# Kernel tuning notes

Hardware: AMD Instinct MI355X
Metric: run time of the kernel (lower is better)

The kernel has to match this reference:

```python
import jax, jax.numpy as jnp
import numpy as np

HEADS = 8


def setup_inputs() -> dict:
    key = jax.random.key(0)
    ks = jax.random.split(key, 12)
    B, H, W, C = 2, 128, 256, 256
    inner = C  # num_heads * dim_head = 8 * 32

    def p(k, shape):
        return jax.random.normal(k, shape, dtype=jnp.float32) * 0.02

    return {
        "x": jax.random.normal(ks[0], (B, H * W, C), dtype=jnp.float32),
        "Wq_h": p(ks[1], (C, inner)),
        "Wk_h": p(ks[2], (C, inner)),
        "Wv_h": p(ks[3], (C, inner)),
        "Wo_h": p(ks[4], (inner, C)),
        "bo_h": p(ks[5], (C,)),
        "Wq_w": p(ks[6], (C, inner)),
        "Wk_w": p(ks[7], (C, inner)),
        "Wv_w": p(ks[8], (C, inner)),
        "Wo_w": p(ks[9], (inner, C)),
        "bo_w": p(ks[10], (C,)),
        "h": H,
        "w": W,
    }


def reference(x, Wq_h, Wk_h, Wv_h, Wo_h, bo_h, Wq_w, Wk_w, Wv_w, Wo_w, bo_w, h, w):
    b, n, c = x.shape
    heads = HEADS
    d = Wq_h.shape[1] // heads  # dim_head
    scale = d ** -0.5
    xs = x.reshape(b, h, w, c)  # [B,H,W,C]

    def proj(Wm):
        # [B,H,W,heads,d]
        return (xs @ Wm).reshape(b, h, w, heads, d)

    # --- height-axis attention: each column attends across all rows ---
    q, k, v = proj(Wq_h), proj(Wk_h), proj(Wv_h)
    s = jnp.einsum('bxwnd,bywnd->bwnxy', q, k) * scale  # [B,W,heads,H,H]
    a = jax.nn.softmax(s, axis=-1)
    oh = jnp.einsum('bwnxy,bywnd->bxwnd', a, v).reshape(b, h, w, heads * d)
    oh = oh @ Wo_h + bo_h

    # --- width-axis attention: each row attends across all columns ---
    q, k, v = proj(Wq_w), proj(Wk_w), proj(Wv_w)
    s = jnp.einsum('bhxnd,bhynd->bhnxy', q, k) * scale  # [B,H,heads,W,W]
    a = jax.nn.softmax(s, axis=-1)
    ow = jnp.einsum('bhnxy,bhynd->bhxnd', a, v).reshape(b, h, w, heads * d)
    ow = ow @ Wo_w + bo_w

    return (oh + ow).reshape(b, n, c)
```

## Files before the change

### kernel.cpp

```cpp
#include <hip/hip_runtime.h>
#include <hip/hip_bf16.h>
#include <stdint.h>

typedef unsigned short u16;
typedef short bf16x8 __attribute__((ext_vector_type(8)));
typedef float f32x4  __attribute__((ext_vector_type(4)));
typedef float f32x16 __attribute__((ext_vector_type(16)));
typedef unsigned int u32x4 __attribute__((ext_vector_type(4)));

__device__ __forceinline__ u16 f2bf(float f) {
    uint32_t u = __builtin_bit_cast(uint32_t, f);
    u += 0x7fffu + ((u >> 16) & 1u);
    return (u16)(u >> 16);
}

#if __has_builtin(__builtin_amdgcn_exp2f)
#define EXP2(x) __builtin_amdgcn_exp2f(x)
#else
extern "C" __device__ float __ocml_native_exp2_f32(float);
#define EXP2(x) __ocml_native_exp2_f32(x)
#endif

#define MM 65536
#define CC 256

#define QSCALE (1.4426950408889634f * 0.17677669529663687f)

__device__ __forceinline__ int perm_h(int t) {
    return ((t >> 15) << 15) | ((t & 127) << 8) | ((t >> 7) & 255);
}


__global__ void prep_kernel(
    const float* __restrict__ Wq_h, const float* __restrict__ Wk_h, const float* __restrict__ Wv_h,
    const float* __restrict__ Wo_h, const float* __restrict__ bo_h,
    const float* __restrict__ Wq_w, const float* __restrict__ Wk_w, const float* __restrict__ Wv_w,
    const float* __restrict__ Wo_w, const float* __restrict__ bo_w,
    u16* __restrict__ Wh_t, u16* __restrict__ Ww_t,
    u16* __restrict__ Woh_t, u16* __restrict__ Wow_t,
    u16* __restrict__ Wocat, float* __restrict__ bias)
{
    const int tid = blockIdx.x * 256 + threadIdx.x;
    const int nth = gridDim.x * 256;

    for (int i = tid; i < 768 * 256; i += nth) {
        int n = i >> 8, kk = i & 255;
        int which = n >> 8, nn = n & 255;
        const float* Wsh = (which == 0) ? Wq_h : (which == 1) ? Wk_h : Wv_h;
        const float* Wsw = (which == 0) ? Wq_w : (which == 1) ? Wk_w : Wv_w;
        Wh_t[i] = f2bf(Wsh[kk * 256 + nn]);
        Ww_t[i] = f2bf(Wsw[kk * 256 + nn]);
    }
    for (int i = tid; i < 256 * 256; i += nth) {
        int n = i >> 8, k = i & 255;
        Woh_t[i] = f2bf(Wo_h[k * 256 + n]);
        Wow_t[i] = f2bf(Wo_w[k * 256 + n]);
    }
    for (int i = tid; i < 256 * 512; i += nth) {
        int n = i >> 9, k = i & 511;
        float v = (k < 256) ? Wo_h[k * 256 + n] : Wo_w[(k - 256) * 256 + n];
        Wocat[i] = f2bf(v);
    }
    for (int i = tid; i < 256; i += nth) bias[i] = bo_h[i] + bo_w[i];
}

__global__ __launch_bounds__(256) void xcvt_kernel(const float* __restrict__ x, u16* __restrict__ xb)
{
    int i = blockIdx.x * 256 + threadIdx.x;
    const int nth = gridDim.x * 256;
    const int total = MM * 256 / 8;
    for (; i < total; i += nth) {
        const float* ap = x + (size_t)i * 8;
        float4 f0 = *(const float4*)ap;
        float4 f1 = *(const float4*)(ap + 4);
        u16 o[8] = { f2bf(f0.x), f2bf(f0.y), f2bf(f0.z), f2bf(f0.w),
                     f2bf(f1.x), f2bf(f1.y), f2bf(f1.z), f2bf(f1.w) };
        *(int4*)(xb + (size_t)i * 8) = *(const int4*)o;
    }
}

template<int PH, int XB>
__global__ __launch_bounds__(256) void gemm_qk_kernel(
    const float* __restrict__ x, const u16* __restrict__ xb, const u16* __restrict__ Bt,
    u16* __restrict__ Qb, u16* __restrict__ Kb)
{
    constexpr int S = PH ? 128 : 256;
    constexpr int L = PH ? 7 : 8;
    const int K = 256;
    __shared__ u16 sh[128 * 128];
    u16* As = sh;
    u16* Bs = sh + 128 * 64;
    const int tid = threadIdx.x;
    const int lane = tid & 63, wave = tid >> 6;
    const int wm = wave & 1, wn = wave >> 1;
    const int l15 = lane & 15, lq = lane >> 4;

    const int id = blockIdx.x;
    const int xcd = id & 7, wq = id >> 3;
    const int mt = xcd * 64 + (wq >> 2), nt = wq & 3;
    const int m0 = mt * 128, n0 = nt * 128;

    f32x4 acc[4][4];
#pragma unroll
    for (int i = 0; i < 4; i++)
#pragma unroll
        for (int j = 0; j < 4; j++)
#pragma unroll
            for (int t = 0; t < 4; t++) acc[i][j][t] = 0.0f;

    for (int kt = 0; kt < K; kt += 64) {
        __syncthreads();
#pragma unroll
        for (int i = 0; i < 4; i++) {
            int cid = i * 256 + tid;
            int r = cid >> 3, sc = cid & 7;
            int gk = kt + ((sc ^ (r & 7)) << 3);
            int rm = PH ? perm_h(m0 + r) : (m0 + r);
            if constexpr (XB) {
                *(int4*)(As + (size_t)cid * 8) = *(const int4*)(xb + (size_t)rm * 256 + gk);
            } else {
                const float* ap = x + (size_t)rm * 256 + gk;
                float4 f0 = *(const float4*)ap;
                float4 f1 = *(const float4*)(ap + 4);
                u16 o[8] = { f2bf(f0.x), f2bf(f0.y), f2bf(f0.z), f2bf(f0.w),
                             f2bf(f1.x), f2bf(f1.y), f2bf(f1.z), f2bf(f1.w) };
                *(int4*)(As + (size_t)cid * 8) = *(const int4*)o;
            }
            *(int4*)(Bs + (size_t)cid * 8) = *(const int4*)(Bt + (size_t)(n0 + r) * K + gk);
        }
        __syncthreads();
#pragma unroll
        for (int ks = 0; ks < 2; ks++) {
            bf16x8 af[4], bfr[4];
#pragma unroll
            for (int i = 0; i < 4; i++) {
                int row = wm * 64 + i * 16 + l15;
                int ca  = ks * 4 + lq;
                af[i]  = *(const bf16x8*)(As + row * 64 + ((ca ^ (row & 7)) << 3));
                int nn  = wn * 64 + i * 16 + l15;
                bfr[i] = *(const bf16x8*)(Bs + nn * 64 + ((ca ^ (nn & 7)) << 3));
            }
#pragma unroll
            for (int i = 0; i < 4; i++)
#pragma unroll
                for (int j = 0; j < 4; j++)
                    acc[i][j] = __builtin_amdgcn_mfma_f32_16x16x32_bf16(af[i], bfr[j], acc[i][j], 0, 0, 0);
        }
    }

    const float scale = (nt < 2) ? (float)QSCALE : 1.0f;
    __syncthreads();
#pragma unroll
    for (int i = 0; i < 4; i++)
#pragma unroll
        for (int j = 0; j < 4; j++)
#pragma unroll
            for (int r = 0; r < 4; r++) {
                int row = wm * 64 + i * 16 + lq * 4 + r;
                int col = wn * 64 + j * 16 + l15;
                sh[row * 128 + (col ^ ((row & 7) << 3))] = f2bf(acc[i][j][r] * scale);
            }
    __syncthreads();

    u16* dstb = (nt < 2) ? Qb : Kb;
    const int head = (nt * 4 + wave) & 7;
    const int gi = m0 >> L;
    const int seqbase = m0 & (S - 1);
    u16* dst = dstb + ((size_t)(gi * 8 + head) * S + seqbase) * 32;
    const int ln_ = lane & 31, lh_ = lane >> 5;
#pragma unroll
    for (int qt = 0; qt < 4; qt++)
#pragma unroll
        for (int half = 0; half < 2; half++) {
            int row  = qt * 32 + ln_;
            int colb = wave * 32 + half * 16 + lh_ * 8;
            int4 v = *(const int4*)(sh + row * 128 + (colb ^ ((row & 7) << 3)));
            *(int4*)(dst + qt * 1024 + half * 512 + lane * 8) = v;
        }
}

template<int PH, int XB>
__global__ __launch_bounds__(256) void gemm_vt_kernel(
    const u16* __restrict__ Wt, const float* __restrict__ x, const u16* __restrict__ xb,
    u16* __restrict__ Vb)
{
    constexpr int S = PH ? 128 : 256;
    const int K = 256;
    __shared__ u16 sh[128 * 128];
    u16* As = sh;
    u16* Bs = sh + 128 * 64;
    const int tid = threadIdx.x;
    const int lane = tid & 63, wave = tid >> 6;
    const int wm = wave & 1, wn = wave >> 1;
    const int l15 = lane & 15, lq = lane >> 4;
    const int m0 = blockIdx.y * 128, n0 = blockIdx.x * 128;

    f32x4 acc[4][4];
#pragma unroll
    for (int i = 0; i < 4; i++)
#pragma unroll
        for (int j = 0; j < 4; j++)
#pragma unroll
            for (int t = 0; t < 4; t++) acc[i][j][t] = 0.0f;

    for (int kt = 0; kt < K; kt += 64) {
        __syncthreads();
#pragma unroll
        for (int i = 0; i < 4; i++) {
            int cid = i * 256 + tid;
            int r = cid >> 3, sc = cid & 7;
            int gk = kt + ((sc ^ (r & 7)) << 3);
            *(int4*)(As + (size_t)cid * 8) = *(const int4*)(Wt + (size_t)(m0 + r) * K + gk);
            int cm = PH ? perm_h(n0 + r) : (n0 + r);
            if constexpr (XB) {
                *(int4*)(Bs + (size_t)cid * 8) = *(const int4*)(xb + (size_t)cm * 256 + gk);
            } else {
                const float* bp = x + (size_t)cm * 256 + gk;
                float4 f0 = *(const float4*)bp;
                float4 f1 = *(const float4*)(bp + 4);
                u16 o[8] = { f2bf(f0.x), f2bf(f0.y), f2bf(f0.z), f2bf(f0.w),
                             f2bf(f1.x), f2bf(f1.y), f2bf(f1.z), f2bf(f1.w) };
                *(int4*)(Bs + (size_t)cid * 8) = *(const int4*)o;
            }
        }
        __syncthreads();
#pragma unroll
        for (int ks = 0; ks < 2; ks++) {
            bf16x8 af[4], bfr[4];
#pragma unroll
            for (int i = 0; i < 4; i++) {
                int row = wm * 64 + i * 16 + l15;
                int ca  = ks * 4 + lq;
                af[i]  = *(const bf16x8*)(As + row * 64 + ((ca ^ (row & 7)) << 3));
                int nn  = wn * 64 + i * 16 + l15;
                bfr[i] = *(const bf16x8*)(Bs + nn * 64 + ((ca ^ (nn & 7)) << 3));
            }
#pragma unroll
            for (int i = 0; i < 4; i++)
#pragma unroll
                for (int j = 0; j < 4; j++)
                    acc[i][j] = __builtin_amdgcn_mfma_f32_16x16x32_bf16(af[i], bfr[j], acc[i][j], 0, 0, 0);
        }
    }

    __syncthreads();
#pragma unroll
    for (int i = 0; i < 4; i++)
#pragma unroll
        for (int j = 0; j < 4; j++)
#pragma unroll
            for (int r = 0; r < 4; r++) {
                int row = wm * 64 + i * 16 + lq * 4 + r;
                int col = wn * 64 + j * 16 + l15;
                sh[row * 128 + (col ^ ((row & 7) << 3))] = f2bf(acc[i][j][r]);
            }
    __syncthreads();

    const int gi = n0 >> (PH ? 7 : 8);
    const int seqbase = n0 & (S - 1);
    const int head = (m0 >> 5) + wave;
    u16* dst = Vb + ((size_t)(gi * 8 + head) * S + seqbase) * 32;
    const int ln_ = lane & 31, lh_ = lane >> 5;
#pragma unroll
    for (int cl = 0; cl < 4; cl++)
#pragma unroll
        for (int half = 0; half < 2; half++) {
            int row  = wave * 32 + ln_;
            int colb = cl * 32 + half * 16 + lh_ * 8;
            int4 v = *(const int4*)(sh + row * 128 + (colb ^ ((row & 7) << 3)));
            *(int4*)(dst + cl * 1024 + half * 512 + lane * 8) = v;
        }
}

__global__ __launch_bounds__(256) void gemm_out_fused_kernel(
    const u16* __restrict__ Ah, const u16* __restrict__ Aw,
    const u16* __restrict__ Bcat, float* __restrict__ Cout, const float* __restrict__ bias)
{
    const int K = 512, N = 256;
    __shared__ u16 As[128 * 64];
    __shared__ u16 Bs[128 * 64];
    const int tid = threadIdx.x;
    const int lane = tid & 63, wave = tid >> 6;
    const int wm = wave & 1, wn = wave >> 1;
    const int l15 = lane & 15, lq = lane >> 4;

    const int id = blockIdx.x;
    const int xcd = id & 7, wq = id >> 3;
    const int mt = xcd * 64 + (wq >> 1), nt = wq & 1;
    const int m0 = mt * 128, n0 = nt * 128;

    f32x4 acc[4][4];
#pragma unroll
    for (int i = 0; i < 4; i++)
#pragma unroll
        for (int j = 0; j < 4; j++)
#pragma unroll
            for (int t = 0; t < 4; t++) acc[i][j][t] = 0.0f;

    for (int kt = 0; kt < K; kt += 64) {
        __syncthreads();
        const u16* Abase = (kt < 256) ? Ah : Aw;
        int koff = kt & 255;
#pragma unroll
        for (int i = 0; i < 4; i++) {
            int cid = i * 256 + tid;
            int r = cid >> 3, sc = cid & 7;
            int gs = (sc ^ (r & 7)) << 3;
            *(int4*)(As + (size_t)cid * 8) = *(const int4*)(Abase + (size_t)(m0 + r) * 256 + koff + gs);
            *(int4*)(Bs + (size_t)cid * 8) = *(const int4*)(Bcat + (size_t)(n0 + r) * K + kt + gs);
        }
        __syncthreads();
#pragma unroll
        for (int ks = 0; ks < 2; ks++) {
            bf16x8 af[4], bfr[4];
#pragma unroll
            for (int i = 0; i < 4; i++) {
                int row = wm * 64 + i * 16 + l15;
                int ca  = ks * 4 + lq;
                af[i]  = *(const bf16x8*)(As + row * 64 + ((ca ^ (row & 7)) << 3));
                int nn  = wn * 64 + i * 16 + l15;
                bfr[i] = *(const bf16x8*)(Bs + nn * 64 + ((ca ^ (nn & 7)) << 3));
            }
#pragma unroll
            for (int i = 0; i < 4; i++)
#pragma unroll
                for (int j = 0; j < 4; j++)
                    acc[i][j] = __builtin_amdgcn_mfma_f32_16x16x32_bf16(af[i], bfr[j], acc[i][j], 0, 0, 0);
        }
    }
#pragma unroll
    for (int i = 0; i < 4; i++)
#pragma unroll
        for (int j = 0; j < 4; j++)
#pragma unroll
            for (int r = 0; r < 4; r++) {
                int row = m0 + wm * 64 + i * 16 + lq * 4 + r;
                int col = n0 + wn * 64 + j * 16 + l15;
                Cout[(size_t)row * N + col] = acc[i][j][r] + bias[col];
            }
}

template<int MODE>
__global__ __launch_bounds__(256) void gemm_out_kernel(
    const u16* __restrict__ A16, const u16* __restrict__ Bt,
    float* __restrict__ Cout, const float* __restrict__ bias)
{
    const int K = 256, N = 256;
    __shared__ u16 As[128 * 64];
    __shared__ u16 Bs[128 * 64];
    const int tid = threadIdx.x;
    const int lane = tid & 63, wave = tid >> 6;
    const int wm = wave & 1, wn = wave >> 1;
    const int l15 = lane & 15, lq = lane >> 4;
    const int m0 = blockIdx.y * 128, n0 = blockIdx.x * 128;

    f32x4 acc[4][4];
#pragma unroll
    for (int i = 0; i < 4; i++)
#pragma unroll
        for (int j = 0; j < 4; j++)
#pragma unroll
            for (int t = 0; t < 4; t++) acc[i][j][t] = 0.0f;

    for (int kt = 0; kt < K; kt += 64) {
        __syncthreads();
#pragma unroll
        for (int i = 0; i < 4; i++) {
            int cid = i * 256 + tid;
            int r = cid >> 3, sc = cid & 7;
            int gk = kt + ((sc ^ (r & 7)) << 3);
            *(int4*)(As + (size_t)cid * 8) = *(const int4*)(A16 + (size_t)(m0 + r) * K + gk);
            *(int4*)(Bs + (size_t)cid * 8) = *(const int4*)(Bt + (size_t)(n0 + r) * K + gk);
        }
        __syncthreads();
#pragma unroll
        for (int ks = 0; ks < 2; ks++) {
            bf16x8 af[4], bfr[4];
#pragma unroll
            for (int i = 0; i < 4; i++) {
                int row = wm * 64 + i * 16 + l15;
                int ca  = ks * 4 + lq;
                af[i]  = *(const bf16x8*)(As + row * 64 + ((ca ^ (row & 7)) << 3));
                int nn  = wn * 64 + i * 16 + l15;
                bfr[i] = *(const bf16x8*)(Bs + nn * 64 + ((ca ^ (nn & 7)) << 3));
            }
#pragma unroll
            for (int i = 0; i < 4; i++)
#pragma unroll
                for (int j = 0; j < 4; j++)
                    acc[i][j] = __builtin_amdgcn_mfma_f32_16x16x32_bf16(af[i], bfr[j], acc[i][j], 0, 0, 0);
        }
    }
#pragma unroll
    for (int i = 0; i < 4; i++)
#pragma unroll
        for (int j = 0; j < 4; j++)
#pragma unroll
            for (int r = 0; r < 4; r++) {
                int row = m0 + wm * 64 + i * 16 + lq * 4 + r;
                int col = n0 + wn * 64 + j * 16 + l15;
                size_t idx = (size_t)row * N + col;
                if (MODE == 1) Cout[idx] = acc[i][j][r] + bias[col];
                else           Cout[idx] += acc[i][j][r];
            }
}

template<int S, int PH, int NT>
__global__ __launch_bounds__(NT) void attn_kernel(
    const u16* __restrict__ Qb, const u16* __restrict__ Kb,
    const u16* __restrict__ Vb, u16* __restrict__ att)
{
    constexpr int NC = S / 32;
    const int tid = threadIdx.x;
    const int lane = tid & 63;
    const int wave = tid >> 6;
    const int ln = lane & 31;
    const int lh = lane >> 5;

    const int bid = blockIdx.x;
    const int head = bid & 7;
    const int gi = bid >> 3;
    const int qs = wave * 32;
    const int g = gi * 8 + head;

    const u16* Qg = Qb + (size_t)g * S * 32;
    const u16* Kg = Kb + (size_t)g * S * 32;
    const u16* Vg = Vb + (size_t)g * S * 32;

    const u16* qp = Qg + (qs >> 5) * 1024 + lane * 8;
    bf16x8 bq0 = *(const bf16x8*)qp;
    bf16x8 bq1 = *(const bf16x8*)(qp + 512);

    f32x16 kz;
#pragma unroll
    for (int t = 0; t < 16; t++) kz[t] = 0.0f;
    asm("" : "+v"(kz));

    float rs[4] = {0.0f, 0.0f, 0.0f, 0.0f};
    f32x16 oacc;
#pragma unroll
    for (int t = 0; t < 16; t++) oacc[t] = 0.0f;

    const u16* kp0 = Kg + lane * 8;
    const u16* vp0 = Vg + lane * 8;
    bf16x8 ak0 = *(const bf16x8*)kp0;
    bf16x8 ak1 = *(const bf16x8*)(kp0 + 512);
    bf16x8 bv0 = *(const bf16x8*)vp0;
    bf16x8 bv1 = *(const bf16x8*)(vp0 + 512);

    for (int c = 0; c < NC; c++) {
        f32x16 z = __builtin_amdgcn_mfma_f32_32x32x16_bf16(ak0, bq0, kz, 0, 0, 0);
        z = __builtin_amdgcn_mfma_f32_32x32x16_bf16(ak1, bq1, z, 0, 0, 0);

        int cn = (c + 1 < NC) ? c + 1 : c;
        const u16* kp = kp0 + cn * 1024;
        const u16* vp = vp0 + cn * 1024;
        bf16x8 nk0 = *(const bf16x8*)kp;
        bf16x8 nk1 = *(const bf16x8*)(kp + 512);
        bf16x8 nv0 = *(const bf16x8*)vp;
        bf16x8 nv1 = *(const bf16x8*)(vp + 512);

        asm("" : "+v"(z));
        float p[16];
#pragma unroll
        for (int r = 0; r < 16; r++) { p[r] = EXP2(z[r]); rs[r & 3] += p[r]; }

        unsigned w[8];
#pragma unroll
        for (int t = 0; t < 8; t++) {
            unsigned d;
            asm("v_cvt_pk_bf16_f32 %0, %1, %2" : "=v"(d) : "v"(p[2 * t]), "v"(p[2 * t + 1]));
            w[t] = d;
        }
        auto s0 = __builtin_amdgcn_permlane32_swap(w[0], w[2], false, false);
        auto s1 = __builtin_amdgcn_permlane32_swap(w[1], w[3], false, false);
        auto s2 = __builtin_amdgcn_permlane32_swap(w[4], w[6], false, false);
        auto s3 = __builtin_amdgcn_permlane32_swap(w[5], w[7], false, false);
        u32x4 a0 = { (unsigned)s0[0], (unsigned)s1[0], (unsigned)s0[1], (unsigned)s1[1] };
        u32x4 a1 = { (unsigned)s2[0], (unsigned)s3[0], (unsigned)s2[1], (unsigned)s3[1] };
        bf16x8 pa0 = __builtin_bit_cast(bf16x8, a0);
        bf16x8 pa1 = __builtin_bit_cast(bf16x8, a1);

        oacc = __builtin_amdgcn_mfma_f32_32x32x16_bf16(pa0, bv0, oacc, 0, 0, 0);
        oacc = __builtin_amdgcn_mfma_f32_32x32x16_bf16(pa1, bv1, oacc, 0, 0, 0);

        ak0 = nk0; ak1 = nk1; bv0 = nv0; bv1 = nv1;
    }

    float rsum = (rs[0] + rs[1]) + (rs[2] + rs[3]);
    rsum += __shfl_xor(rsum, 32);
    float inv = 1.0f / rsum;
#pragma unroll
    for (int r = 0; r < 16; r++) {
        int row = (r & 3) + ((r >> 2) << 3) + (lh << 2);
        float is = __shfl(inv, row);
        int seq = qs + row;
        int m = PH ? ((gi >> 8) * 32768 + seq * 256 + (gi & 255))
                   : (gi * 256 + seq);
        att[(size_t)m * 256 + head * 32 + ln] = f2bf(oacc[r] * is);
    }
}

extern "C" void kernel_launch(void* const* d_in, const int* in_sizes, int n_in,
                              void* d_out, int out_size, void* d_ws, size_t ws_size,
                              hipStream_t stream)
{
    (void)in_sizes; (void)n_in; (void)out_size;
    const float* x    = (const float*)d_in[0];
    const float* Wq_h = (const float*)d_in[1];
    const float* Wk_h = (const float*)d_in[2];
    const float* Wv_h = (const float*)d_in[3];
    const float* Wo_h = (const float*)d_in[4];
    const float* bo_h = (const float*)d_in[5];
    const float* Wq_w = (const float*)d_in[6];
    const float* Wk_w = (const float*)d_in[7];
    const float* Wv_w = (const float*)d_in[8];
    const float* Wo_w = (const float*)d_in[9];
    const float* bo_w = (const float*)d_in[10];

    const size_t NB = (size_t)MM * 256;
    u16* Qb   = (u16*)d_ws;
    u16* Kb   = Qb + NB;
    u16* Vb   = Kb + NB;
    u16* attb = Vb + NB;
    u16* xb   = attb + NB;
    const size_t WT = (size_t)2 * 768 * 256 + (size_t)2 * 256 * 256 + (size_t)256 * 512 + 512;
    const bool use_xb = ws_size >= (5 * NB + WT) * sizeof(u16);
    u16* wp = use_xb ? (xb + NB) : xb;
    u16* Wh_t  = wp;
    u16* Ww_t  = Wh_t + 768 * 256;
    u16* Woh_t = Ww_t + 768 * 256;
    u16* Wow_t = Woh_t + 256 * 256;
    u16* Wocat = Wow_t + 256 * 256;
    float* bias = (float*)(Wocat + 256 * 512);

    prep_kernel<<<512, 256, 0, stream>>>(Wq_h, Wk_h, Wv_h, Wo_h, bo_h,
                                         Wq_w, Wk_w, Wv_w, Wo_w, bo_w,
                                         Wh_t, Ww_t, Woh_t, Wow_t, Wocat, bias);
    if (use_xb)
        xcvt_kernel<<<8192, 256, 0, stream>>>(x, xb);

    if (use_xb) {
        gemm_qk_kernel<1, 1><<<2048, 256, 0, stream>>>(x, xb, Wh_t, Qb, Kb);
        gemm_vt_kernel<1, 1><<<dim3(512, 2), 256, 0, stream>>>(Wh_t + 512 * 256, x, xb, Vb);
        attn_kernel<128, 1, 256><<<4096, 256, 0, stream>>>(Qb, Kb, Vb, attb);

        gemm_qk_kernel<0, 1><<<2048, 256, 0, stream>>>(x, xb, Ww_t, Qb, Kb);
        gemm_vt_kernel<0, 1><<<dim3(512, 2), 256, 0, stream>>>(Ww_t + 512 * 256, x, xb, Vb);
        attn_kernel<256, 0, 512><<<2048, 512, 0, stream>>>(Qb, Kb, Vb, xb);

        gemm_out_fused_kernel<<<1024, 256, 0, stream>>>(attb, xb, Wocat,
                                                        (float*)d_out, bias);
    } else {
        gemm_qk_kernel<1, 0><<<2048, 256, 0, stream>>>(x, xb, Wh_t, Qb, Kb);
        gemm_vt_kernel<1, 0><<<dim3(512, 2), 256, 0, stream>>>(Wh_t + 512 * 256, x, xb, Vb);
        attn_kernel<128, 1, 256><<<4096, 256, 0, stream>>>(Qb, Kb, Vb, attb);
        gemm_out_kernel<1><<<dim3(2, 512), 256, 0, stream>>>(attb, Woh_t, (float*)d_out, bias);

        gemm_qk_kernel<0, 0><<<2048, 256, 0, stream>>>(x, xb, Ww_t, Qb, Kb);
        gemm_vt_kernel<0, 0><<<dim3(512, 2), 256, 0, stream>>>(Ww_t + 512 * 256, x, xb, Vb);
        attn_kernel<256, 0, 512><<<2048, 512, 0, stream>>>(Qb, Kb, Vb, attb);
        gemm_out_kernel<2><<<dim3(2, 512), 256, 0, stream>>>(attb, Wow_t, (float*)d_out, nullptr);
    }
}
```

Measured before the change: 322.8 us.

## Double-buffer GEMM tiles with direct global-to-LDS async loads

In the QK, VT (bf16 input path) and fused output-projection GEMMs, tile staging now uses global_load_lds builtins that write 16-byte chunks straight into LDS, bypassing registers. Shared memory is double-buffered so the next K-tile is fetched while MFMAs run on the current one, with one barrier per iteration instead of two. This targets exposed global-load latency in these projection GEMMs. The cost is doubled LDS per block, which may lower occupancy, and correctness depends on the barrier covering completion of the asynchronous LDS writes.

```diff
diff --git a/kernel.cpp b/kernel.cpp
--- a/kernel.cpp
+++ b/kernel.cpp
@@ -20,6 +20,13 @@
 extern "C" __device__ float __ocml_native_exp2_f32(float);
 #define EXP2(x) __ocml_native_exp2_f32(x)
 #endif
+
+__device__ __forceinline__ void gl_lds16(const u16* g, u16* l) {
+    __builtin_amdgcn_global_load_lds(
+        (__attribute__((address_space(1))) void*)(g),
+        (__attribute__((address_space(3))) void*)(l),
+        16, 0, 0);
+}
 
 #define MM 65536
 #define CC 256
@@ -87,9 +94,7 @@
     constexpr int S = PH ? 128 : 256;
     constexpr int L = PH ? 7 : 8;
     const int K = 256;
-    __shared__ u16 sh[128 * 128];
-    u16* As = sh;
-    u16* Bs = sh + 128 * 64;
+    __shared__ u16 sh[XB ? 32768 : 16384];
     const int tid = threadIdx.x;
     const int lane = tid & 63, wave = tid >> 6;
     const int wm = wave & 1, wn = wave >> 1;
@@ -108,48 +113,74 @@
 #pragma unroll
             for (int t = 0; t < 4; t++) acc[i][j][t] = 0.0f;
 
-    for (int kt = 0; kt < K; kt += 64) {
+    auto mma_tile = [&](const u16* As, const u16* Bs) {
+#pragma unroll
+        for (int ks = 0; ks < 2; ks++) {
+            bf16x8 af[4], bfr[4];
+#pragma unroll
+            for (int i = 0; i < 4; i++) {
+                int row = wm * 64 + i * 16 + l15;
+                int ca  = ks * 4 + lq;
+                af[i]  = *(const bf16x8*)(As + row * 64 + ((ca ^ (row & 7)) << 3));
+                int nn  = wn * 64 + i * 16 + l15;
+                bfr[i] = *(const bf16x8*)(Bs + nn * 64 + ((ca ^ (nn & 7)) << 3));
+            }
+#pragma unroll
+            for (int i = 0; i < 4; i++)
+#pragma unroll
+                for (int j = 0; j < 4; j++)
+                    acc[i][j] = __builtin_amdgcn_mfma_f32_16x16x32_bf16(af[i], bfr[j], acc[i][j], 0, 0, 0);
+        }
+    };
+
+    if constexpr (XB) {
+        u16* As_[2] = { sh,        sh + 16384 };
+        u16* Bs_[2] = { sh + 8192, sh + 24576 };
+        auto stage = [&](int kt, int buf) {
+#pragma unroll
+            for (int i = 0; i < 4; i++) {
+                int cid = i * 256 + tid;
+                int r = cid >> 3, sc = cid & 7;
+                int gk = kt + ((sc ^ (r & 7)) << 3);
+                int rm = PH ? perm_h(m0 + r) : (m0 + r);
+                gl_lds16(xb + (size_t)rm * 256 + gk, As_[buf] + cid * 8);
+                gl_lds16(Bt + (size_t)(n0 + r) * K + gk, Bs_[buf] + cid * 8);
+            }
+        };
+        stage(0, 0);
         __syncthreads();
 #pragma unroll
-        for (int i = 0; i < 4; i++) {
-            int cid = i * 256 + tid;
-            int r = cid >> 3, sc = cid & 7;
-            int gk = kt + ((sc ^ (r & 7)) << 3);
-            int rm = PH ? perm_h(m0 + r) : (m0 + r);
-            if constexpr (XB) {
-                *(int4*)(As + (size_t)cid * 8) = *(const int4*)(xb + (size_t)rm * 256 + gk);
-            } else {
+        for (int t = 0; t < 4; t++) {
+            if (t + 1 < 4) stage((t + 1) * 64, (t + 1) & 1);
+            mma_tile(As_[t & 1], Bs_[t & 1]);
+            __syncthreads();
+        }
+    } else {
+        u16* As = sh;
+        u16* Bs = sh + 8192;
+        for (int kt = 0; kt < K; kt += 64) {
+            __syncthreads();
+#pragma unroll
+            for (int i = 0; i < 4; i++) {
+                int cid = i * 256 + tid;
+                int r = cid >> 3, sc = cid & 7;
+                int gk = kt + ((sc ^ (r & 7)) << 3);
+                int rm = PH ? perm_h(m0 + r) : (m0 + r);
                 const float* ap = x + (size_t)rm * 256 + gk;
                 float4 f0 = *(const float4*)ap;
                 float4 f1 = *(const float4*)(ap + 4);
                 u16 o[8] = { f2bf(f0.x), f2bf(f0.y), f2bf(f0.z), f2bf(f0.w),
                              f2bf(f1.x), f2bf(f1.y), f2bf(f1.z), f2bf(f1.w) };
                 *(int4*)(As + (size_t)cid * 8) = *(const int4*)o;
-            }
-            *(int4*)(Bs + (size_t)cid * 8) = *(const int4*)(Bt + (size_t)(n0 + r) * K + gk);
+                *(int4*)(Bs + (size_t)cid * 8) = *(const int4*)(Bt + (size_t)(n0 + r) * K + gk);
+            }
+            __syncthreads();
+            mma_tile(As, Bs);
         }
         __syncthreads();
-#pragma unroll
-        for (int ks = 0; ks < 2; ks++) {
-            bf16x8 af[4], bfr[4];
-#pragma unroll
-            for (int i = 0; i < 4; i++) {
-                int row = wm * 64 + i * 16 + l15;
-                int ca  = ks * 4 + lq;
-                af[i]  = *(const bf16x8*)(As + row * 64 + ((ca ^ (row & 7)) << 3));
-                int nn  = wn * 64 + i * 16 + l15;
-                bfr[i] = *(const bf16x8*)(Bs + nn * 64 + ((ca ^ (nn & 7)) << 3));
-            }
-#pragma unroll
-            for (int i = 0; i < 4; i++)
-#pragma unroll
-                for (int j = 0; j < 4; j++)
-                    acc[i][j] = __builtin_amdgcn_mfma_f32_16x16x32_bf16(af[i], bfr[j], acc[i][j], 0, 0, 0);
-        }
     }
 
     const float scale = (nt < 2) ? (float)QSCALE : 1.0f;
-    __syncthreads();
 #pragma unroll
     for (int i = 0; i < 4; i++)
 #pragma unroll
@@ -186,9 +217,7 @@
 {
     constexpr int S = PH ? 128 : 256;
     const int K = 256;
-    __shared__ u16 sh[128 * 128];
-    u16* As = sh;
-    u16* Bs = sh + 128 * 64;
+    __shared__ u16 sh[XB ? 32768 : 16384];
     const int tid = threadIdx.x;
     const int lane = tid & 63, wave = tid >> 6;
     const int wm = wave & 1, wn = wave >> 1;
@@ -203,18 +232,60 @@
 #pragma unroll
             for (int t = 0; t < 4; t++) acc[i][j][t] = 0.0f;
 
-    for (int kt = 0; kt < K; kt += 64) {
+    auto mma_tile = [&](const u16* As, const u16* Bs) {
+#pragma unroll
+        for (int ks = 0; ks < 2; ks++) {
+            bf16x8 af[4], bfr[4];
+#pragma unroll
+            for (int i = 0; i < 4; i++) {
+                int row = wm * 64 + i * 16 + l15;
+                int ca  = ks * 4 + lq;
+                af[i]  = *(const bf16x8*)(As + row * 64 + ((ca ^ (row & 7)) << 3));
+                int nn  = wn * 64 + i * 16 + l15;
+                bfr[i] = *(const bf16x8*)(Bs + nn * 64 + ((ca ^ (nn & 7)) << 3));
+            }
+#pragma unroll
+            for (int i = 0; i < 4; i++)
+#pragma unroll
+                for (int j = 0; j < 4; j++)
+                    acc[i][j] = __builtin_amdgcn_mfma_f32_16x16x32_bf16(af[i], bfr[j], acc[i][j], 0, 0, 0);
+        }
+    };
+
+    if constexpr (XB) {
+        u16* As_[2] = { sh,        sh + 16384 };
+        u16* Bs_[2] = { sh + 8192, sh + 24576 };
+        auto stage = [&](int kt, int buf) {
+#pragma unroll
+            for (int i = 0; i < 4; i++) {
+                int cid = i * 256 + tid;
+                int r = cid >> 3, sc = cid & 7;
+                int gk = kt + ((sc ^ (r & 7)) << 3);
+                gl_lds16(Wt + (size_t)(m0 + r) * K + gk, As_[buf] + cid * 8);
+                int cm = PH ? perm_h(n0 + r) : (n0 + r);
+                gl_lds16(xb + (size_t)cm * 256 + gk, Bs_[buf] + cid * 8);
+            }
+        };
+        stage(0, 0);
         __syncthreads();
 #pragma unroll
-        for (int i = 0; i < 4; i++) {
-            int cid = i * 256 + tid;
-            int r = cid >> 3, sc = cid & 7;
-            int gk = kt + ((sc ^ (r & 7)) << 3);
-            *(int4*)(As + (size_t)cid * 8) = *(const int4*)(Wt + (size_t)(m0 + r) * K + gk);
-            int cm = PH ? perm_h(n0 + r) : (n0 + r);
-            if constexpr (XB) {
-                *(int4*)(Bs + (size_t)cid * 8) = *(const int4*)(xb + (size_t)cm * 256 + gk);
-            } else {
+        for (int t = 0; t < 4; t++) {
+            if (t + 1 < 4) stage((t + 1) * 64, (t + 1) & 1);
+            mma_tile(As_[t & 1], Bs_[t & 1]);
+            __syncthreads();
+        }
+    } else {
+        u16* As = sh;
+        u16* Bs = sh + 8192;
+        for (int kt = 0; kt < K; kt += 64) {
+            __syncthreads();
+#pragma unroll
+            for (int i = 0; i < 4; i++) {
+                int cid = i * 256 + tid;
+                int r = cid >> 3, sc = cid & 7;
+                int gk = kt + ((sc ^ (r & 7)) << 3);
+                *(int4*)(As + (size_t)cid * 8) = *(const int4*)(Wt + (size_t)(m0 + r) * K + gk);
+                int cm = PH ? perm_h(n0 + r) : (n0 + r);
                 const float* bp = x + (size_t)cm * 256 + gk;
                 float4 f0 = *(const float4*)bp;
                 float4 f1 = *(const float4*)(bp + 4);
@@ -222,8 +293,86 @@
                              f2bf(f1.x), f2bf(f1.y), f2bf(f1.z), f2bf(f1.w) };
                 *(int4*)(Bs + (size_t)cid * 8) = *(const int4*)o;
             }
+            __syncthreads();
+            mma_tile(As, Bs);
         }
         __syncthreads();
+    }
+
+#pragma unroll
+    for (int i = 0; i < 4; i++)
+#pragma unroll
+        for (int j = 0; j < 4; j++)
+#pragma unroll
+            for (int r = 0; r < 4; r++) {
+                int row = wm * 64 + i * 16 + lq * 4 + r;
+                int col = wn * 64 + j * 16 + l15;
+                sh[row * 128 + (col ^ ((row & 7) << 3))] = f2bf(acc[i][j][r]);
+            }
+    __syncthreads();
+
+    const int gi = n0 >> (PH ? 7 : 8);
+    const int seqbase = n0 & (S - 1);
+    const int head = (m0 >> 5) + wave;
+    u16* dst = Vb + ((size_t)(gi * 8 + head) * S + seqbase) * 32;
+    const int ln_ = lane & 31, lh_ = lane >> 5;
+#pragma unroll
+    for (int cl = 0; cl < 4; cl++)
+#pragma unroll
+        for (int half = 0; half < 2; half++) {
+            int row  = wave * 32 + ln_;
+            int colb = cl * 32 + half * 16 + lh_ * 8;
+            int4 v = *(const int4*)(sh + row * 128 + (colb ^ ((row & 7) << 3)));
+            *(int4*)(dst + cl * 1024 + half * 512 + lane * 8) = v;
+        }
+}
+
+__global__ __launch_bounds__(256) void gemm_out_fused_kernel(
+    const u16* __restrict__ Ah, const u16* __restrict__ Aw,
+    const u16* __restrict__ Bcat, float* __restrict__ Cout, const float* __restrict__ bias)
+{
+    const int K = 512, N = 256;
+    __shared__ u16 sh[32768];
+    const int tid = threadIdx.x;
+    const int lane = tid & 63, wave = tid >> 6;
+    const int wm = wave & 1, wn = wave >> 1;
+    const int l15 = lane & 15, lq = lane >> 4;
+
+    const int id = blockIdx.x;
+    const int xcd = id & 7, wq = id >> 3;
+    const int mt = xcd * 64 + (wq >> 1), nt = wq & 1;
+    const int m0 = mt * 128, n0 = nt * 128;
+
+    f32x4 acc[4][4];
+#pragma unroll
+    for (int i = 0; i < 4; i++)
+#pragma unroll
+        for (int j = 0; j < 4; j++)
+#pragma unroll
+            for (int t = 0; t < 4; t++) acc[i][j][t] = 0.0f;
+
+    u16* As_[2] = { sh,        sh + 16384 };
+    u16* Bs_[2] = { sh + 8192, sh + 24576 };
+    auto stage = [&](int kt, int buf) {
+        const u16* Abase = (kt < 256) ? Ah : Aw;
+        int koff = kt & 255;
+#pragma unroll
+        for (int i = 0; i < 4; i++) {
+            int cid = i * 256 + tid;
+            int r = cid >> 3, sc = cid & 7;
+            int gs = (sc ^ (r & 7)) << 3;
+            gl_lds16(Abase + (size_t)(m0 + r) * 256 + koff + gs, As_[buf] + cid * 8);
+            gl_lds16(Bcat + (size_t)(n0 + r) * K + kt + gs, Bs_[buf] + cid * 8);
+        }
+    };
+
+    stage(0, 0);
+    __syncthreads();
+#pragma unroll
+    for (int t = 0; t < 8; t++) {
+        if (t + 1 < 8) stage((t + 1) * 64, (t + 1) & 1);
+        const u16* As = As_[t & 1];
+        const u16* Bs = Bs_[t & 1];
 #pragma unroll
         for (int ks = 0; ks < 2; ks++) {
             bf16x8 af[4], bfr[4];
@@ -241,92 +390,7 @@
                 for (int j = 0; j < 4; j++)
                     acc[i][j] = __builtin_amdgcn_mfma_f32_16x16x32_bf16(af[i], bfr[j], acc[i][j], 0, 0, 0);
         }
-    }
-
-    __syncthreads();
-#pragma unroll
-    for (int i = 0; i < 4; i++)
-#pragma unroll
-        for (int j = 0; j < 4; j++)
-#pragma unroll
-            for (int r = 0; r < 4; r++) {
-                int row = wm * 64 + i * 16 + lq * 4 + r;
-                int col = wn * 64 + j * 16 + l15;
-                sh[row * 128 + (col ^ ((row & 7) << 3))] = f2bf(acc[i][j][r]);
-            }
-    __syncthreads();
-
-    const int gi = n0 >> (PH ? 7 : 8);
-    const int seqbase = n0 & (S - 1);
-    const int head = (m0 >> 5) + wave;
-    u16* dst = Vb + ((size_t)(gi * 8 + head) * S + seqbase) * 32;
-    const int ln_ = lane & 31, lh_ = lane >> 5;
-#pragma unroll
-    for (int cl = 0; cl < 4; cl++)
-#pragma unroll
-        for (int half = 0; half < 2; half++) {
-            int row  = wave * 32 + ln_;
-            int colb = cl * 32 + half * 16 + lh_ * 8;
-            int4 v = *(const int4*)(sh + row * 128 + (colb ^ ((row & 7) << 3)));
-            *(int4*)(dst + cl * 1024 + half * 512 + lane * 8) = v;
-        }
-}
-
-__global__ __launch_bounds__(256) void gemm_out_fused_kernel(
-    const u16* __restrict__ Ah, const u16* __restrict__ Aw,
-    const u16* __restrict__ Bcat, float* __restrict__ Cout, const float* __restrict__ bias)
-{
-    const int K = 512, N = 256;
-    __shared__ u16 As[128 * 64];
-    __shared__ u16 Bs[128 * 64];
-    const int tid = threadIdx.x;
-    const int lane = tid & 63, wave = tid >> 6;
-    const int wm = wave & 1, wn = wave >> 1;
-    const int l15 = lane & 15, lq = lane >> 4;
-
-    const int id = blockIdx.x;
-    const int xcd = id & 7, wq = id >> 3;
-    const int mt = xcd * 64 + (wq >> 1), nt = wq & 1;
-    const int m0 = mt * 128, n0 = nt * 128;
-
-    f32x4 acc[4][4];
-#pragma unroll
-    for (int i = 0; i < 4; i++)
-#pragma unroll
-        for (int j = 0; j < 4; j++)
-#pragma unroll
-            for (int t = 0; t < 4; t++) acc[i][j][t] = 0.0f;
-
-    for (int kt = 0; kt < K; kt += 64) {
         __syncthreads();
-        const u16* Abase = (kt < 256) ? Ah : Aw;
-        int koff = kt & 255;
-#pragma unroll
-        for (int i = 0; i < 4; i++) {
-            int cid = i * 256 + tid;
-            int r = cid >> 3, sc = cid & 7;
-            int gs = (sc ^ (r & 7)) << 3;
-            *(int4*)(As + (size_t)cid * 8) = *(const int4*)(Abase + (size_t)(m0 + r) * 256 + koff + gs);
-            *(int4*)(Bs + (size_t)cid * 8) = *(const int4*)(Bcat + (size_t)(n0 + r) * K + kt + gs);
-        }
-        __syncthreads();
-#pragma unroll
-        for (int ks = 0; ks < 2; ks++) {
-            bf16x8 af[4], bfr[4];
-#pragma unroll
-            for (int i = 0; i < 4; i++) {
-                int row = wm * 64 + i * 16 + l15;
-                int ca  = ks * 4 + lq;
-                af[i]  = *(const bf16x8*)(As + row * 64 + ((ca ^ (row & 7)) << 3));
-                int nn  = wn * 64 + i * 16 + l15;
-                bfr[i] = *(const bf16x8*)(Bs + nn * 64 + ((ca ^ (nn & 7)) << 3));
-            }
-#pragma unroll
-            for (int i = 0; i < 4; i++)
-#pragma unroll
-                for (int j = 0; j < 4; j++)
-                    acc[i][j] = __builtin_amdgcn_mfma_f32_16x16x32_bf16(af[i], bfr[j], acc[i][j], 0, 0, 0);
-        }
     }
 #pragma unroll
     for (int i = 0; i < 4; i++)
```

After: 318.6 us. About the same (-1.3%).
